# Performance work log

Hardware: AMD Instinct MI355X
Metric: run time of the kernel (lower is better)

## Reference

```python
import jax, jax.numpy as jnp
import numpy as np

D = 768           # input_dim == slot_dim
H, DH = 8, 64     # encoder attention heads / head dim (x-transformers defaults)
INNER = 4 * D     # ff_mult=4 GLU inner dim
EPS = 1e-8
N_ITERS = 3
SCALE = D ** -0.5


def _ln(x, g, b):
    m = jnp.mean(x, axis=-1, keepdims=True)
    v = jnp.var(x, axis=-1, keepdims=True)
    return (x - m) / jnp.sqrt(v + 1e-5) * g + b


def setup_inputs() -> dict:
    key = jax.random.key(0)
    ks = jax.random.split(key, 16)
    w = lambda i, shape, s=0.02: jax.random.normal(ks[i], shape, jnp.float32) * s
    return dict(
        x=jax.random.normal(ks[0], (32, 1024, D), jnp.float32),
        noise=jax.random.normal(ks[1], (32, 16, D), jnp.float32),
        init_mu=jax.random.normal(ks[2], (D,), jnp.float32),
        init_log_sigma=w(3, (D,), 0.05),
        Wk=w(4, (D, D)), Wv=w(5, (D, D)), Wq=w(6, (D, D)),
        ni_g=jnp.ones(D), ni_b=jnp.zeros(D),       # norm_input
        ns_g=jnp.ones(D), ns_b=jnp.zeros(D),       # norm_slots
        nica_g=jnp.ones(D), nica_b=jnp.zeros(D),   # norm_ica
        ln1_g=jnp.ones(D), ln1_b=jnp.zeros(D),     # encoder attn pre-norm
        Wq_a=w(7, (D, H * DH)), Wk_a=w(8, (D, H * DH)),
        Wv_a=w(9, (D, H * DH)), Wo_a=w(10, (H * DH, D)),
        ln2_g=jnp.ones(D), ln2_b=jnp.zeros(D),     # encoder ff pre-norm
        W1=w(11, (D, 2 * INNER)), W2=w(12, (INNER, D)),
        lnf_g=jnp.ones(D), lnf_b=jnp.zeros(D),     # encoder final norm
    )


def _inv_cross_attn(q, k, v):
    # softmax over the SLOT axis (dim i), then renormalize over keys j
    dots = jnp.einsum('bid,bjd->bij', q, k) * SCALE
    attn = jax.nn.softmax(dots, axis=1) + EPS
    attn = attn / jnp.sum(attn, axis=-1, keepdims=True)
    updates = jnp.einsum('bjd,bij->bid', v, attn)
    return updates, attn


def _encoder(h, ln1_g, ln1_b, Wq_a, Wk_a, Wv_a, Wo_a, ln2_g, ln2_b, W1, W2, lnf_g, lnf_b):
    b, n, _ = h.shape
    a = _ln(h, ln1_g, ln1_b)
    q = (a @ Wq_a).reshape(b, n, H, DH)
    k = (a @ Wk_a).reshape(b, n, H, DH)
    v = (a @ Wv_a).reshape(b, n, H, DH)
    scores = jnp.einsum('bihd,bjhd->bhij', q, k) * (DH ** -0.5)
    p = jax.nn.softmax(scores, axis=-1)
    o = jnp.einsum('bhij,bjhd->bihd', p, v).reshape(b, n, H * DH)
    h = h + o @ Wo_a
    f = _ln(h, ln2_g, ln2_b)
    u, g = jnp.split(f @ W1, 2, axis=-1)
    h = h + (u * jax.nn.silu(g)) @ W2
    return _ln(h, lnf_g, lnf_b)


def reference(x, noise, init_mu, init_log_sigma, Wk, Wv, Wq,
              ni_g, ni_b, ns_g, ns_b, nica_g, nica_b,
              ln1_g, ln1_b, Wq_a, Wk_a, Wv_a, Wo_a,
              ln2_g, ln2_b, W1, W2, lnf_g, lnf_b):
    xn = _ln(x, ni_g, ni_b)
    k = xn @ Wk
    v = xn @ Wv
    slots = init_mu + jnp.exp(init_log_sigma) * noise  # [b, n_slots, d]

    def step(slots):
        q = _ln(slots, ns_g, ns_b) @ Wq
        updates, attn = _inv_cross_attn(q, k, v)
        slots = _ln(slots + updates, nica_g, nica_b)
        slots = _encoder(slots, ln1_g, ln1_b, Wq_a, Wk_a, Wv_a, Wo_a,
                         ln2_g, ln2_b, W1, W2, lnf_g, lnf_b)
        return slots, attn

    for _ in range(N_ITERS):
        slots, _ = step(slots)
    slots, attn = step(slots)
    attn_map = jnp.transpose(attn, (0, 2, 1))  # b n hw -> b hw n
    return slots, attn_map
```

## Files before the change

### kernel.cpp

```cpp
#include <hip/hip_runtime.h>
#include <hip/hip_bf16.h>
#include <stdint.h>

typedef _Float16 f16;
typedef __attribute__((ext_vector_type(8))) _Float16 f16x8;
typedef __attribute__((ext_vector_type(4))) _Float16 f16x4;
typedef __attribute__((ext_vector_type(4))) float f32x4;

#define GLOBAL_AS __attribute__((address_space(1)))
#define LDS_AS __attribute__((address_space(3)))

#define D_DIM 768
#define NTOK 1024
#define NSLOT 16
#define NB 32
#define NTOT (NB*NTOK)
#define HDIM 512
#define INNER 3072
#define SCALE_D 0.03608439182435161f
#define SCALE_H 0.125f

template<int OUT>
__global__ __launch_bounds__(256) void mgemm64_k(
    const f16* __restrict__ A, const f16* __restrict__ Bt,
    void* __restrict__ Cout, int M, int N, int K, int Kc)
{
  __shared__ __align__(16) f16 As[64*128];
  __shared__ __align__(16) f16 Bs[64*128];
  const int tid = threadIdx.x;
  const int lane = tid & 63;
  const int wave = tid >> 6;
  const int m0 = blockIdx.x*64, n0 = blockIdx.y*64;
  const int kbeg = blockIdx.z * Kc;
  const int wm = (wave>>1)*32, wn = (wave&1)*32;
  const int quad = lane>>4, l16 = lane&15;

  const int sr = tid>>2;
  const int sc = (tid&3)*8;
  const f16* gA = A  + (size_t)(m0+sr)*K + kbeg + sc;
  const f16* gB = Bt + (size_t)(n0+sr)*K + kbeg + sc;
  LDS_AS f16* lA = (LDS_AS f16*)&As[(size_t)tid*8];
  LDS_AS f16* lB = (LDS_AS f16*)&Bs[(size_t)tid*8];

  const f16* fA0 = &As[(wm + l16)*32 + quad*8];
  const f16* fB0 = &Bs[(wn + l16)*32 + quad*8];

  f32x4 acc[2][2] = {};

  for (int k0 = 0; k0 < Kc; k0 += 128){
    #pragma unroll
    for (int p=0;p<4;++p){
      __builtin_amdgcn_global_load_lds((const GLOBAL_AS void*)(gA + k0 + p*32),
                                       (LDS_AS void*)(lA + (size_t)p*2048), 16, 0, 0);
      __builtin_amdgcn_global_load_lds((const GLOBAL_AS void*)(gB + k0 + p*32),
                                       (LDS_AS void*)(lB + (size_t)p*2048), 16, 0, 0);
    }
    __syncthreads();
    #pragma unroll
    for (int p=0;p<4;++p){
      f16x8 a0 = *(const f16x8*)(fA0 + p*2048);
      f16x8 a1 = *(const f16x8*)(fA0 + p*2048 + 16*32);
      f16x8 b0 = *(const f16x8*)(fB0 + p*2048);
      f16x8 b1 = *(const f16x8*)(fB0 + p*2048 + 16*32);
      acc[0][0] = __builtin_amdgcn_mfma_f32_16x16x32_f16(a0,b0,acc[0][0],0,0,0);
      acc[0][1] = __builtin_amdgcn_mfma_f32_16x16x32_f16(a0,b1,acc[0][1],0,0,0);
      acc[1][0] = __builtin_amdgcn_mfma_f32_16x16x32_f16(a1,b0,acc[1][0],0,0,0);
      acc[1][1] = __builtin_amdgcn_mfma_f32_16x16x32_f16(a1,b1,acc[1][1],0,0,0);
    }
    __syncthreads();
  }
  #pragma unroll
  for (int mt=0;mt<2;++mt){
    #pragma unroll
    for (int nt=0;nt<2;++nt){
      int gm = m0 + wm + mt*16 + quad*4;
      int gn = n0 + wn + nt*16 + l16;
      #pragma unroll
      for (int r=0;r<4;++r){
        float c = acc[mt][nt][r];
        size_t idx = (size_t)(gm+r)*N + gn;
        if (OUT==0)      ((float*)Cout)[idx] = c;
        else if (OUT==1) ((f16*)Cout)[idx] = (f16)c;
        else             atomicAdd(&((float*)Cout)[idx], c);
      }
    }
  }
}

__global__ __launch_bounds__(256) void w1glu_k(
    const f16* __restrict__ A, const f16* __restrict__ W1T,
    f16* __restrict__ act, int M)
{
  __shared__ __align__(16) f16 As[64*128];
  __shared__ __align__(16) f16 Bu[64*128];
  __shared__ __align__(16) f16 Bg[64*128];
  const int K = 768;
  const int tid = threadIdx.x;
  const int lane = tid & 63;
  const int wave = tid >> 6;
  const int m0 = blockIdx.x*64, n0 = blockIdx.y*64;
  const int wm = (wave>>1)*32, wn = (wave&1)*32;
  const int quad = lane>>4, l16 = lane&15;

  const int sr = tid>>2;
  const int sc = (tid&3)*8;
  const f16* gA  = A   + (size_t)(m0+sr)*K + sc;
  const f16* gBu = W1T + (size_t)(n0+sr)*K + sc;
  const f16* gBg = W1T + (size_t)(3072+n0+sr)*K + sc;
  LDS_AS f16* lA  = (LDS_AS f16*)&As[(size_t)tid*8];
  LDS_AS f16* lBu = (LDS_AS f16*)&Bu[(size_t)tid*8];
  LDS_AS f16* lBg = (LDS_AS f16*)&Bg[(size_t)tid*8];

  const f16* fA0 = &As[(wm + l16)*32 + quad*8];
  const f16* fU0 = &Bu[(wn + l16)*32 + quad*8];
  const f16* fG0 = &Bg[(wn + l16)*32 + quad*8];

  f32x4 accU[2][2] = {};
  f32x4 accG[2][2] = {};

  for (int k0 = 0; k0 < K; k0 += 128){
    #pragma unroll
    for (int p=0;p<4;++p){
      __builtin_amdgcn_global_load_lds((const GLOBAL_AS void*)(gA  + k0 + p*32),
                                       (LDS_AS void*)(lA  + (size_t)p*2048), 16, 0, 0);
      __builtin_amdgcn_global_load_lds((const GLOBAL_AS void*)(gBu + k0 + p*32),
                                       (LDS_AS void*)(lBu + (size_t)p*2048), 16, 0, 0);
      __builtin_amdgcn_global_load_lds((const GLOBAL_AS void*)(gBg + k0 + p*32),
                                       (LDS_AS void*)(lBg + (size_t)p*2048), 16, 0, 0);
    }
    __syncthreads();
    #pragma unroll
    for (int p=0;p<4;++p){
      f16x8 a0 = *(const f16x8*)(fA0 + p*2048);
      f16x8 a1 = *(const f16x8*)(fA0 + p*2048 + 16*32);
      f16x8 u0 = *(const f16x8*)(fU0 + p*2048);
      f16x8 u1 = *(const f16x8*)(fU0 + p*2048 + 16*32);
      f16x8 g0 = *(const f16x8*)(fG0 + p*2048);
      f16x8 g1 = *(const f16x8*)(fG0 + p*2048 + 16*32);
      accU[0][0] = __builtin_amdgcn_mfma_f32_16x16x32_f16(a0,u0,accU[0][0],0,0,0);
      accU[0][1] = __builtin_amdgcn_mfma_f32_16x16x32_f16(a0,u1,accU[0][1],0,0,0);
      accU[1][0] = __builtin_amdgcn_mfma_f32_16x16x32_f16(a1,u0,accU[1][0],0,0,0);
      accU[1][1] = __builtin_amdgcn_mfma_f32_16x16x32_f16(a1,u1,accU[1][1],0,0,0);
      accG[0][0] = __builtin_amdgcn_mfma_f32_16x16x32_f16(a0,g0,accG[0][0],0,0,0);
      accG[0][1] = __builtin_amdgcn_mfma_f32_16x16x32_f16(a0,g1,accG[0][1],0,0,0);
      accG[1][0] = __builtin_amdgcn_mfma_f32_16x16x32_f16(a1,g0,accG[1][0],0,0,0);
      accG[1][1] = __builtin_amdgcn_mfma_f32_16x16x32_f16(a1,g1,accG[1][1],0,0,0);
    }
    __syncthreads();
  }
  #pragma unroll
  for (int mt=0;mt<2;++mt){
    #pragma unroll
    for (int nt=0;nt<2;++nt){
      int gm = m0 + wm + mt*16 + quad*4;
      int gn = n0 + wn + nt*16 + l16;
      #pragma unroll
      for (int r=0;r<4;++r){
        float u = accU[mt][nt][r];
        float g = accG[mt][nt][r];
        float sg = g / (1.0f + __expf(-g));
        act[(size_t)(gm+r)*INNER + gn] = (f16)(u*sg);
      }
    }
  }
}

__global__ __launch_bounds__(256) void dots_k(
    const f16* __restrict__ Q,
    const f16* __restrict__ Xn,
    f16* __restrict__ attn,
    float* __restrict__ rsPart)
{
  __shared__ __align__(16) f16 qf[16*768];
  __shared__ __align__(16) f16 ks[64*128];
  __shared__ float rpart[4][16];
  const int b = blockIdx.x, jt = blockIdx.y;
  const int tid = threadIdx.x;
  const int lane = tid & 63;
  const int w = tid >> 6;
  const int quad = lane>>4, l16 = lane&15;

  #pragma unroll
  for (int c=0;c<6;++c){
    int p = c*256 + tid;
    int ki = p >> 6, qd = (p >> 4) & 3, rw = p & 15;
    f16x8 v = *(const f16x8*)(Q + ((size_t)(b*NSLOT+rw))*D_DIM + ki*32 + qd*8);
    *(f16x8*)&qf[(size_t)p*8] = v;
  }

  const f16* gK = Xn + ((size_t)(b*NTOK + jt*64 + (tid>>2)))*D_DIM + (tid&3)*8;
  LDS_AS f16* lK = (LDS_AS f16*)&ks[(size_t)tid*8];

  f32x4 acc = {};
  for (int it=0; it<6; ++it){
    #pragma unroll
    for (int p=0;p<4;++p)
      __builtin_amdgcn_global_load_lds((const GLOBAL_AS void*)(gK + it*128 + p*32),
                                       (LDS_AS void*)(lK + (size_t)p*2048), 16, 0, 0);
    __syncthreads();
    #pragma unroll
    for (int p=0;p<4;++p){
      f16x8 a  = *(const f16x8*)&qf[(((size_t)(it*4+p)*4 + quad)*16 + l16)*8];
      f16x8 bf = *(const f16x8*)&ks[(size_t)p*2048 + (w*16+l16)*32 + quad*8];
      acc = __builtin_amdgcn_mfma_f32_16x16x32_f16(a, bf, acc, 0, 0, 0);
    }
    __syncthreads();
  }

  float v0 = acc[0]*SCALE_D, v1 = acc[1]*SCALE_D, v2 = acc[2]*SCALE_D, v3 = acc[3]*SCALE_D;
  float mx = fmaxf(fmaxf(v0,v1), fmaxf(v2,v3));
  mx = fmaxf(mx, __shfl_xor(mx, 16));
  mx = fmaxf(mx, __shfl_xor(mx, 32));
  float e0 = __expf(v0-mx), e1 = __expf(v1-mx), e2 = __expf(v2-mx), e3 = __expf(v3-mx);
  float s = e0+e1+e2+e3;
  s += __shfl_xor(s, 16);
  s += __shfl_xor(s, 32);
  float inv = 1.0f/s;
  float a0 = e0*inv + 1e-8f, a1 = e1*inv + 1e-8f, a2 = e2*inv + 1e-8f, a3 = e3*inv + 1e-8f;

  int jcol = jt*64 + w*16 + l16;
  int ibase = b*NSLOT + quad*4;
  attn[(size_t)(ibase+0)*NTOK + jcol] = (f16)a0;
  attn[(size_t)(ibase+1)*NTOK + jcol] = (f16)a1;
  attn[(size_t)(ibase+2)*NTOK + jcol] = (f16)a2;
  attn[(size_t)(ibase+3)*NTOK + jcol] = (f16)a3;

  float t0=a0, t1=a1, t2=a2, t3=a3;
  #pragma unroll
  for (int m=1;m<16;m<<=1){
    t0 += __shfl_xor(t0, m);
    t1 += __shfl_xor(t1, m);
    t2 += __shfl_xor(t2, m);
    t3 += __shfl_xor(t3, m);
  }
  if (l16 == 0){
    rpart[w][quad*4+0] = t0;
    rpart[w][quad*4+1] = t1;
    rpart[w][quad*4+2] = t2;
    rpart[w][quad*4+3] = t3;
  }
  __syncthreads();
  if (tid < 16){
    float ss = rpart[0][tid] + rpart[1][tid] + rpart[2][tid] + rpart[3][tid];
    rsPart[(size_t)((b*16 + jt)<<4) + tid] = ss;
  }
}

__global__ __launch_bounds__(256) void attnv_k(
    const f16* __restrict__ attn,
    const float* __restrict__ rsPart,
    const f16* __restrict__ XnT,
    f16* __restrict__ t_out)
{
  __shared__ __align__(16) f16 Asl[16*128];
  __shared__ __align__(16) f16 Bsl[64*128];
  __shared__ float rsum[16];
  const int b = blockIdx.x, d0 = blockIdx.y*64;
  const int tid = threadIdx.x;
  const int lane = tid & 63;
  const int w = tid >> 6;
  const int quad = lane>>4, l16 = lane&15;

  if (tid < 16){
    float s = 0.f;
    #pragma unroll
    for (int jt=0;jt<16;++jt) s += rsPart[(size_t)((b*16 + jt)<<4) + tid];
    rsum[tid] = s;
  }

  const int pa = tid>>6, ta = tid&63;
  const f16* gA = attn + ((size_t)(b*NSLOT + (ta>>2)))*NTOK + pa*32 + (ta&3)*8;
  LDS_AS f16* lA = (LDS_AS f16*)&Asl[(size_t)pa*512 + ta*8];
  const f16* gB = XnT + ((size_t)(d0 + (tid>>2)))*NTOT + b*NTOK + (tid&3)*8;
  LDS_AS f16* lB = (LDS_AS f16*)&Bsl[(size_t)tid*8];

  f32x4 acc = {};
  for (int it=0; it<8; ++it){
    __builtin_amdgcn_global_load_lds((const GLOBAL_AS void*)(gA + it*128),
                                     (LDS_AS void*)lA, 16, 0, 0);
    #pragma unroll
    for (int p=0;p<4;++p)
      __builtin_amdgcn_global_load_lds((const GLOBAL_AS void*)(gB + it*128 + p*32),
                                       (LDS_AS void*)(lB + (size_t)p*2048), 16, 0, 0);
    __syncthreads();
    #pragma unroll
    for (int p=0;p<4;++p){
      f16x8 a  = *(const f16x8*)&Asl[(size_t)p*512 + l16*32 + quad*8];
      f16x8 bf = *(const f16x8*)&Bsl[(size_t)p*2048 + (w*16+l16)*32 + quad*8];
      acc = __builtin_amdgcn_mfma_f32_16x16x32_f16(a, bf, acc, 0, 0, 0);
    }
    __syncthreads();
  }
  int dcol = d0 + w*16 + l16;
  #pragma unroll
  for (int r=0;r<4;++r){
    int i = quad*4 + r;
    t_out[(size_t)(b*NSLOT + i)*D_DIM + dcol] = (f16)(acc[r] / rsum[i]);
  }
}

__global__ __launch_bounds__(256) void lnw_k(
    const float* __restrict__ X,
    const float* __restrict__ g, const float* __restrict__ bb,
    f16* __restrict__ out)
{
  const int lane = threadIdx.x & 63;
  const size_t row = (size_t)blockIdx.x*4 + (threadIdx.x>>6);
  const float* x = X + row*D_DIM;
  float4 v[3]; float s=0.f, ss=0.f;
  #pragma unroll
  for (int t=0;t<3;++t){
    v[t] = *(const float4*)(x + lane*4 + t*256);
    s  += v[t].x+v[t].y+v[t].z+v[t].w;
    ss += v[t].x*v[t].x+v[t].y*v[t].y+v[t].z*v[t].z+v[t].w*v[t].w;
  }
  #pragma unroll
  for (int m=1;m<64;m<<=1){ s += __shfl_xor(s,m); ss += __shfl_xor(ss,m); }
  float mean = s*(1.0f/768.0f);
  float inv  = rsqrtf(ss*(1.0f/768.0f) - mean*mean + 1e-5f);
  #pragma unroll
  for (int t=0;t<3;++t){
    int c0 = lane*4 + t*256;
    float4 gg = *(const float4*)(g + c0);
    float4 bv = *(const float4*)(bb + c0);
    f16x4 h4;
    h4.x = (f16)((v[t].x-mean)*inv*gg.x + bv.x);
    h4.y = (f16)((v[t].y-mean)*inv*gg.y + bv.y);
    h4.z = (f16)((v[t].z-mean)*inv*gg.z + bv.z);
    h4.w = (f16)((v[t].w-mean)*inv*gg.w + bv.w);
    *(f16x4*)(out + row*D_DIM + c0) = h4;
  }
}

template<bool ADD>
__global__ __launch_bounds__(256) void lnlnw_k(
    const float* __restrict__ X, const float* __restrict__ X2,
    const float* __restrict__ g1, const float* __restrict__ b1,
    const float* __restrict__ g2, const float* __restrict__ b2,
    float* __restrict__ out1, f16* __restrict__ out2)
{
  const int lane = threadIdx.x & 63;
  const size_t row = (size_t)blockIdx.x*4 + (threadIdx.x>>6);
  const float* x = X + row*D_DIM;
  const float* x2 = X2 + row*D_DIM;
  float4 v[3]; float s=0.f, ss=0.f;
  #pragma unroll
  for (int t=0;t<3;++t){
    int c0 = lane*4 + t*256;
    float4 a = *(const float4*)(x + c0);
    if (ADD){
      float4 b = *(const float4*)(x2 + c0);
      a.x+=b.x; a.y+=b.y; a.z+=b.z; a.w+=b.w;
    }
    v[t]=a;
    s  += v[t].x+v[t].y+v[t].z+v[t].w;
    ss += v[t].x*v[t].x+v[t].y*v[t].y+v[t].z*v[t].z+v[t].w*v[t].w;
  }
  #pragma unroll
  for (int m=1;m<64;m<<=1){ s += __shfl_xor(s,m); ss += __shfl_xor(ss,m); }
  float mean = s*(1.0f/768.0f);
  float inv  = rsqrtf(ss*(1.0f/768.0f) - mean*mean + 1e-5f);
  float y[3][4]; float s2=0.f, ss2=0.f;
  #pragma unroll
  for (int t=0;t<3;++t){
    int c0 = lane*4 + t*256;
    float4 gg = *(const float4*)(g1 + c0);
    float4 bv = *(const float4*)(b1 + c0);
    y[t][0] = (v[t].x-mean)*inv*gg.x + bv.x;
    y[t][1] = (v[t].y-mean)*inv*gg.y + bv.y;
    y[t][2] = (v[t].z-mean)*inv*gg.z + bv.z;
    y[t][3] = (v[t].w-mean)*inv*gg.w + bv.w;
    float4 o = { y[t][0], y[t][1], y[t][2], y[t][3] };
    *(float4*)(out1 + row*D_DIM + c0) = o;
    s2  += y[t][0]+y[t][1]+y[t][2]+y[t][3];
    ss2 += y[t][0]*y[t][0]+y[t][1]*y[t][1]+y[t][2]*y[t][2]+y[t][3]*y[t][3];
  }
  #pragma unroll
  for (int m=1;m<64;m<<=1){ s2 += __shfl_xor(s2,m); ss2 += __shfl_xor(ss2,m); }
  float mean2 = s2*(1.0f/768.0f);
  float inv2  = rsqrtf(ss2*(1.0f/768.0f) - mean2*mean2 + 1e-5f);
  #pragma unroll
  for (int t=0;t<3;++t){
    int c0 = lane*4 + t*256;
    float4 gg = *(const float4*)(g2 + c0);
    float4 bv = *(const float4*)(b2 + c0);
    f16x4 h4;
    h4.x = (f16)((y[t][0]-mean2)*inv2*gg.x + bv.x);
    h4.y = (f16)((y[t][1]-mean2)*inv2*gg.y + bv.y);
    h4.z = (f16)((y[t][2]-mean2)*inv2*gg.z + bv.z);
    h4.w = (f16)((y[t][3]-mean2)*inv2*gg.w + bv.w);
    *(f16x4*)(out2 + row*D_DIM + c0) = h4;
  }
}

__global__ __launch_bounds__(256) void slotsinit_k(
    const float* __restrict__ noise, const float* __restrict__ mu,
    const float* __restrict__ ls,
    const float* __restrict__ nsg, const float* __restrict__ nsb,
    float* __restrict__ slots, f16* __restrict__ tmp2)
{
  const int lane = threadIdx.x & 63;
  const size_t row = (size_t)blockIdx.x*4 + (threadIdx.x>>6);
  float4 v[3]; float s=0.f, ss=0.f;
  #pragma unroll
  for (int t=0;t<3;++t){
    int c0 = lane*4 + t*256;
    float4 nz = *(const float4*)(noise + row*D_DIM + c0);
    float4 m4 = *(const float4*)(mu + c0);
    float4 l4 = *(const float4*)(ls + c0);
    v[t].x = m4.x + __expf(l4.x)*nz.x;
    v[t].y = m4.y + __expf(l4.y)*nz.y;
    v[t].z = m4.z + __expf(l4.z)*nz.z;
    v[t].w = m4.w + __expf(l4.w)*nz.w;
    *(float4*)(slots + row*D_DIM + c0) = v[t];
    s  += v[t].x+v[t].y+v[t].z+v[t].w;
    ss += v[t].x*v[t].x+v[t].y*v[t].y+v[t].z*v[t].z+v[t].w*v[t].w;
  }
  #pragma unroll
  for (int m=1;m<64;m<<=1){ s += __shfl_xor(s,m); ss += __shfl_xor(ss,m); }
  float mean = s*(1.0f/768.0f);
  float inv  = rsqrtf(ss*(1.0f/768.0f) - mean*mean + 1e-5f);
  #pragma unroll
  for (int t=0;t<3;++t){
    int c0 = lane*4 + t*256;
    float4 gg = *(const float4*)(nsg + c0);
    float4 bv = *(const float4*)(nsb + c0);
    f16x4 h4;
    h4.x = (f16)((v[t].x-mean)*inv*gg.x + bv.x);
    h4.y = (f16)((v[t].y-mean)*inv*gg.y + bv.y);
    h4.z = (f16)((v[t].z-mean)*inv*gg.z + bv.z);
    h4.w = (f16)((v[t].w-mean)*inv*gg.w + bv.w);
    *(f16x4*)(tmp2 + row*D_DIM + c0) = h4;
  }
}

__global__ __launch_bounds__(256) void encattn_k(
    const f16* __restrict__ QA, const f16* __restrict__ KA,
    const f16* __restrict__ VA, int QSTR,
    f16* __restrict__ O)
{
  __shared__ float qs[16][68], ks[16][68], vs[16][68], ps[16][20];
  const int b = blockIdx.x, h = blockIdx.y;
  const int tid = threadIdx.x;
  {
    int i = tid>>4, dd=(tid&15)*4;
    size_t base = ((size_t)(b*NSLOT+i))*QSTR + h*64 + dd;
    f16x4 uq = *(const f16x4*)(QA + base);
    f16x4 uk = *(const f16x4*)(KA + base);
    f16x4 uv = *(const f16x4*)(VA + base);
    float4 fq = { (float)uq.x, (float)uq.y, (float)uq.z, (float)uq.w };
    float4 fk = { (float)uk.x, (float)uk.y, (float)uk.z, (float)uk.w };
    float4 fv = { (float)uv.x, (float)uv.y, (float)uv.z, (float)uv.w };
    *(float4*)&qs[i][dd]=fq; *(float4*)&ks[i][dd]=fk; *(float4*)&vs[i][dd]=fv;
  }
  __syncthreads();
  {
    int i = tid>>4, j = tid&15;
    float s=0.f;
    #pragma unroll 8
    for (int d=0; d<64; ++d) s += qs[i][d]*ks[j][d];
    ps[i][j] = s*SCALE_H;
  }
  __syncthreads();
  if (tid < 16){
    int i = tid;
    float mx=-1e30f;
    #pragma unroll
    for (int j=0;j<16;++j) mx = fmaxf(mx, ps[i][j]);
    float sm=0.f;
    #pragma unroll
    for (int j=0;j<16;++j){ float e=__expf(ps[i][j]-mx); ps[i][j]=e; sm+=e; }
    float inv=1.0f/sm;
    #pragma unroll
    for (int j=0;j<16;++j) ps[i][j]*=inv;
  }
  __syncthreads();
  {
    int i = tid>>4, dq=(tid&15)*4;
    float a0=0,a1=0,a2=0,a3=0;
    #pragma unroll
    for (int j=0;j<16;++j){
      float p = ps[i][j];
      a0+=p*vs[j][dq+0]; a1+=p*vs[j][dq+1]; a2+=p*vs[j][dq+2]; a3+=p*vs[j][dq+3];
    }
    size_t base = ((size_t)(b*NSLOT+i))*HDIM + h*64 + dq;
    O[base+0]=(f16)a0; O[base+1]=(f16)a1; O[base+2]=(f16)a2; O[base+3]=(f16)a3;
  }
}

__global__ __launch_bounds__(256) void transp_k(
    const f16* __restrict__ in, f16* __restrict__ out, int R, int C)
{
  __shared__ f16 T[64][72];
  const int m0 = blockIdx.x*64, d0 = blockIdx.y*64;
  const int tid = threadIdx.x;
  {
    int r = tid>>2, c = (tid&3)*16;
    const f16* p = in + (size_t)(m0+r)*C + d0 + c;
    *(f16x8*)&T[r][c]   = *(const f16x8*)p;
    *(f16x8*)&T[r][c+8] = *(const f16x8*)(p+8);
  }
  __syncthreads();
  {
    int dd = tid>>2, mq = (tid&3)*16;
    f16 v[16];
    #pragma unroll
    for (int e=0;e<16;++e) v[e] = T[mq+e][dd];
    f16* p = out + (size_t)(d0+dd)*R + m0 + mq;
    *(f16x8*)p     = *(f16x8*)&v[0];
    *(f16x8*)(p+8) = *(f16x8*)&v[8];
  }
}

__global__ __launch_bounds__(256) void prep_k(
    const float* __restrict__ Wv,   const float* __restrict__ Wq_a,
    const float* __restrict__ Wk_a, const float* __restrict__ Wv_a,
    const float* __restrict__ Wo_a, const float* __restrict__ W1,
    const float* __restrict__ W2,   const float* __restrict__ Wk,
    const float* __restrict__ Wq,
    f16* __restrict__ WvT, f16* __restrict__ WqkvT, f16* __restrict__ WoaT,
    f16* __restrict__ W1T, f16* __restrict__ W2T,
    f16* __restrict__ Wkf, f16* __restrict__ Wqf)
{
  __shared__ float t[32][33];
  int bid = blockIdx.x;
  const float* src; f16* dst; int R, C; bool tr = true;
  if      (bid < 576)  {              src=Wv;   dst=WvT;             R=768;  C=768; }
  else if (bid < 960)  { bid-=576;    src=Wq_a; dst=WqkvT;           R=768;  C=512; }
  else if (bid < 1344) { bid-=960;    src=Wk_a; dst=WqkvT+512*768;   R=768;  C=512; }
  else if (bid < 1728) { bid-=1344;   src=Wv_a; dst=WqkvT+1024*768;  R=768;  C=512; }
  else if (bid < 2112) { bid-=1728;   src=Wo_a; dst=WoaT;            R=512;  C=768; }
  else if (bid < 6720) { bid-=2112;   src=W1;   dst=W1T;             R=768;  C=6144; }
  else if (bid < 9024) { bid-=6720;   src=W2;   dst=W2T;             R=3072; C=768; }
  else if (bid < 9600) { bid-=9024;   src=Wk;   dst=Wkf;             R=768;  C=768; tr=false; }
  else                 { bid-=9600;   src=Wq;   dst=Wqf;             R=768;  C=768; tr=false; }
  const int tpr = C/32;
  const int r0 = (bid / tpr)*32, c0 = (bid % tpr)*32;
  const int lc = threadIdx.x & 31, g8 = threadIdx.x >> 5;
  if (tr){
    #pragma unroll
    for (int s=0;s<4;++s){
      int r = g8*4 + s;
      t[r][lc] = src[(size_t)(r0+r)*C + c0+lc];
    }
    __syncthreads();
    #pragma unroll
    for (int s=0;s<4;++s){
      int c = g8*4 + s;
      dst[(size_t)(c0+c)*R + r0+lc] = (f16)t[lc][c];
    }
  } else {
    #pragma unroll
    for (int s=0;s<4;++s){
      int r = g8*4 + s;
      dst[(size_t)(r0+r)*C + c0+lc] = (f16)src[(size_t)(r0+r)*C + c0+lc];
    }
  }
}

__global__ __launch_bounds__(256) void attnout_k(
    const f16* __restrict__ attn, const float* __restrict__ rsPart,
    float* __restrict__ out)
{
  __shared__ float rsum[16];
  const int bid = blockIdx.x, tid = threadIdx.x;
  const int b = bid >> 6;
  if (tid < 16){
    float s = 0.f;
    #pragma unroll
    for (int jt=0;jt<16;++jt) s += rsPart[(size_t)((b*16+jt)<<4) + tid];
    rsum[tid] = s;
  }
  __syncthreads();
  int idx = bid*256 + tid;
  int i = idx & 15;
  int j = (idx >> 4) & 1023;
  out[idx] = (float)attn[((size_t)(b*NSLOT)+i)*NTOK + j] / rsum[i];
}

extern "C" void kernel_launch(void* const* d_in, const int* in_sizes, int n_in,
                              void* d_out, int out_size, void* d_ws, size_t ws_size,
                              hipStream_t stream) {
  const float* x        = (const float*)d_in[0];
  const float* noise    = (const float*)d_in[1];
  const float* init_mu  = (const float*)d_in[2];
  const float* init_ls  = (const float*)d_in[3];
  const float* Wk       = (const float*)d_in[4];
  const float* Wv       = (const float*)d_in[5];
  const float* Wq       = (const float*)d_in[6];
  const float* ni_g     = (const float*)d_in[7];
  const float* ni_b     = (const float*)d_in[8];
  const float* ns_g     = (const float*)d_in[9];
  const float* ns_b     = (const float*)d_in[10];
  const float* nica_g   = (const float*)d_in[11];
  const float* nica_b   = (const float*)d_in[12];
  const float* ln1_g    = (const float*)d_in[13];
  const float* ln1_b    = (const float*)d_in[14];
  const float* Wq_a     = (const float*)d_in[15];
  const float* Wk_a     = (const float*)d_in[16];
  const float* Wv_a     = (const float*)d_in[17];
  const float* Wo_a     = (const float*)d_in[18];
  const float* ln2_g    = (const float*)d_in[19];
  const float* ln2_b    = (const float*)d_in[20];
  const float* W1       = (const float*)d_in[21];
  const float* W2       = (const float*)d_in[22];
  const float* lnf_g    = (const float*)d_in[23];
  const float* lnf_b    = (const float*)d_in[24];

  char* w = (char*)d_ws;
  size_t off = 0;
  auto alloc = [&](size_t bytes)->char*{
    char* p = w + off; off += (bytes + 255) & ~(size_t)255; return p;
  };
  f16* xn_h  = (f16*)alloc((size_t)NTOT*D_DIM*2);
  f16* xnT_h = (f16*)alloc((size_t)D_DIM*NTOT*2);
  f16* Wkf   = (f16*)alloc((size_t)768*768*2);
  f16* Wqf   = (f16*)alloc((size_t)768*768*2);
  f16* BtQK  = (f16*)alloc((size_t)768*768*2);
  f16* WvT   = (f16*)alloc((size_t)768*768*2);
  f16* WqkvT = (f16*)alloc((size_t)1536*768*2);
  f16* WoaT  = (f16*)alloc((size_t)768*512*2);
  f16* W1T   = (f16*)alloc((size_t)6144*768*2);
  f16* W2T   = (f16*)alloc((size_t)768*3072*2);
  float* slots = (float*)alloc(512*768*4);
  float* hbuf  = (float*)alloc(512*768*4);
  float* upd   = (float*)alloc(512*768*4);
  f16* tmp_h  = (f16*)alloc(512*768*2);
  f16* tmp2_h = (f16*)alloc(512*768*2);
  f16* q_h    = (f16*)alloc(512*768*2);
  f16* t_h    = (f16*)alloc(512*768*2);
  f16* qkv_h  = (f16*)alloc((size_t)512*1536*2);
  f16* o_h    = (f16*)alloc(512*512*2);
  f16* act_h  = (f16*)alloc((size_t)512*3072*2);
  f16* attn_h = (f16*)alloc((size_t)NB*NSLOT*NTOK*2);
  float* rsPart = (float*)alloc((size_t)32*16*16*4);

  prep_k<<<10176, 256, 0, stream>>>(Wv, Wq_a, Wk_a, Wv_a, Wo_a, W1, W2, Wk, Wq,
                                    WvT, WqkvT, WoaT, W1T, W2T, Wkf, Wqf);

  mgemm64_k<1><<<dim3(12, 12, 1), 256, 0, stream>>>(Wkf, Wqf, BtQK, 768, 768, 768, 768);

  lnw_k<<<NTOT/4, 256, 0, stream>>>(x, ni_g, ni_b, xn_h);
  transp_k<<<dim3(NTOT/64, D_DIM/64), 256, 0, stream>>>(xn_h, xnT_h, NTOT, D_DIM);

  slotsinit_k<<<128, 256, 0, stream>>>(noise, init_mu, init_ls, ns_g, ns_b,
                                       slots, tmp2_h);

  for (int it=0; it<4; ++it){
    mgemm64_k<1><<<dim3(8, 12, 1), 256, 0, stream>>>(tmp2_h, BtQK, q_h, 512, 768, 768, 768);
    dots_k<<<dim3(NB, 16), 256, 0, stream>>>(q_h, xn_h, attn_h, rsPart);
    attnv_k<<<dim3(NB, 12), 256, 0, stream>>>(attn_h, rsPart, xnT_h, t_h);
    mgemm64_k<0><<<dim3(8, 12, 1), 256, 0, stream>>>(t_h, WvT, upd, 512, 768, 768, 768);
    lnlnw_k<true><<<128, 256, 0, stream>>>(slots, upd, nica_g, nica_b, ln1_g, ln1_b,
                                           hbuf, tmp_h);
    mgemm64_k<1><<<dim3(8, 24, 1), 256, 0, stream>>>(tmp_h, WqkvT, qkv_h, 512, 1536, 768, 768);
    encattn_k<<<dim3(NB, 8), 256, 0, stream>>>(qkv_h, qkv_h + 512, qkv_h + 1024, 1536, o_h);
    mgemm64_k<2><<<dim3(8, 12, 2), 256, 0, stream>>>(o_h, WoaT, hbuf, 512, 768, 512, 256);
    lnw_k<<<128, 256, 0, stream>>>(hbuf, ln2_g, ln2_b, tmp_h);
    w1glu_k<<<dim3(8, 48), 256, 0, stream>>>(tmp_h, W1T, act_h, 512);
    mgemm64_k<2><<<dim3(8, 12, 4), 256, 0, stream>>>(act_h, W2T, hbuf, 512, 768, 3072, 768);
    float* out1 = (it==3) ? (float*)d_out : slots;
    lnlnw_k<false><<<128, 256, 0, stream>>>(hbuf, nullptr, lnf_g, lnf_b, ns_g, ns_b,
                                            out1, tmp2_h);
  }

  attnout_k<<<NB*NTOK*NSLOT/256, 256, 0, stream>>>(attn_h, rsPart, (float*)d_out + 512*768);
}
```

Baseline: 627.9 us.

## Replace atomic split-K with partial buffers reduced in consumer kernels

All the small slot-side GEMMs now run split-K. Each K-slice writes its fp32 partial to its own buffer instead of using atomicAdd. The partials are summed inside the kernels that consume them (dots, layernorm, encoder attention), which spreads 512-row GEMMs over more blocks and drops the atomics. The cost is extra fp32 partial traffic, more workspace, and changed rounding because the q/qkv intermediates are now fp32 sums rather than fp16.

After: 634.8 us. Within noise of the previous version (+1.1%).

```diff
diff --git a/kernel.cpp b/kernel.cpp
--- a/kernel.cpp
+++ b/kernel.cpp
@@ -17,6 +17,7 @@
 #define NTOT (NB*NTOK)
 #define HDIM 512
 #define INNER 3072
+#define SLOTSZ (512*768)
 #define SCALE_D 0.03608439182435161f
 #define SCALE_H 0.125f
 
@@ -69,6 +70,7 @@
     }
     __syncthreads();
   }
+  const size_t zoff = (size_t)blockIdx.z * M * N;
   #pragma unroll
   for (int mt=0;mt<2;++mt){
     #pragma unroll
@@ -79,9 +81,8 @@
       for (int r=0;r<4;++r){
         float c = acc[mt][nt][r];
         size_t idx = (size_t)(gm+r)*N + gn;
-        if (OUT==0)      ((float*)Cout)[idx] = c;
-        else if (OUT==1) ((f16*)Cout)[idx] = (f16)c;
-        else             atomicAdd(&((float*)Cout)[idx], c);
+        if (OUT==1) ((f16*)Cout)[idx] = (f16)c;
+        else        ((float*)Cout)[zoff + idx] = c;
       }
     }
   }
@@ -166,7 +167,8 @@
 }
 
 __global__ __launch_bounds__(256) void dots_k(
-    const f16* __restrict__ Q,
+    const float* __restrict__ Q0, const float* __restrict__ Q1,
+    const float* __restrict__ Q2,
     const f16* __restrict__ Xn,
     f16* __restrict__ attn,
     float* __restrict__ rsPart)
@@ -184,7 +186,15 @@
   for (int c=0;c<6;++c){
     int p = c*256 + tid;
     int ki = p >> 6, qd = (p >> 4) & 3, rw = p & 15;
-    f16x8 v = *(const f16x8*)(Q + ((size_t)(b*NSLOT+rw))*D_DIM + ki*32 + qd*8);
+    size_t qo = ((size_t)(b*NSLOT+rw))*D_DIM + ki*32 + qd*8;
+    float4 a0 = *(const float4*)(Q0+qo), a1 = *(const float4*)(Q0+qo+4);
+    float4 b0 = *(const float4*)(Q1+qo), b1 = *(const float4*)(Q1+qo+4);
+    float4 c0 = *(const float4*)(Q2+qo), c1 = *(const float4*)(Q2+qo+4);
+    f16x8 v;
+    v[0]=(f16)(a0.x+b0.x+c0.x); v[1]=(f16)(a0.y+b0.y+c0.y);
+    v[2]=(f16)(a0.z+b0.z+c0.z); v[3]=(f16)(a0.w+b0.w+c0.w);
+    v[4]=(f16)(a1.x+b1.x+c1.x); v[5]=(f16)(a1.y+b1.y+c1.y);
+    v[6]=(f16)(a1.z+b1.z+c1.z); v[7]=(f16)(a1.w+b1.w+c1.w);
     *(f16x8*)&qf[(size_t)p*8] = v;
   }
 
@@ -332,27 +342,26 @@
   }
 }
 
-template<bool ADD>
-__global__ __launch_bounds__(256) void lnlnw_k(
-    const float* __restrict__ X, const float* __restrict__ X2,
+__global__ __launch_bounds__(256) void lnln_res_k(
+    const float* __restrict__ S,  const float* __restrict__ U0,
+    const float* __restrict__ U1, const float* __restrict__ U2,
     const float* __restrict__ g1, const float* __restrict__ b1,
     const float* __restrict__ g2, const float* __restrict__ b2,
     float* __restrict__ out1, f16* __restrict__ out2)
 {
   const int lane = threadIdx.x & 63;
   const size_t row = (size_t)blockIdx.x*4 + (threadIdx.x>>6);
-  const float* x = X + row*D_DIM;
-  const float* x2 = X2 + row*D_DIM;
+  const size_t ro = row*D_DIM;
   float4 v[3]; float s=0.f, ss=0.f;
   #pragma unroll
   for (int t=0;t<3;++t){
     int c0 = lane*4 + t*256;
-    float4 a = *(const float4*)(x + c0);
-    if (ADD){
-      float4 b = *(const float4*)(x2 + c0);
-      a.x+=b.x; a.y+=b.y; a.z+=b.z; a.w+=b.w;
-    }
-    v[t]=a;
+    float4 a = *(const float4*)(S + ro + c0);
+    float4 b = *(const float4*)(U0 + ro + c0);
+    float4 c = *(const float4*)(U1 + ro + c0);
+    float4 d = *(const float4*)(U2 + ro + c0);
+    v[t].x = a.x+b.x+c.x+d.x; v[t].y = a.y+b.y+c.y+d.y;
+    v[t].z = a.z+b.z+c.z+d.z; v[t].w = a.w+b.w+c.w+d.w;
     s  += v[t].x+v[t].y+v[t].z+v[t].w;
     ss += v[t].x*v[t].x+v[t].y*v[t].y+v[t].z*v[t].z+v[t].w*v[t].w;
   }
@@ -371,7 +380,7 @@
     y[t][2] = (v[t].z-mean)*inv*gg.z + bv.z;
     y[t][3] = (v[t].w-mean)*inv*gg.w + bv.w;
     float4 o = { y[t][0], y[t][1], y[t][2], y[t][3] };
-    *(float4*)(out1 + row*D_DIM + c0) = o;
+    *(float4*)(out1 + ro + c0) = o;
     s2  += y[t][0]+y[t][1]+y[t][2]+y[t][3];
     ss2 += y[t][0]*y[t][0]+y[t][1]*y[t][1]+y[t][2]*y[t][2]+y[t][3]*y[t][3];
   }
@@ -389,7 +398,107 @@
     h4.y = (f16)((y[t][1]-mean2)*inv2*gg.y + bv.y);
     h4.z = (f16)((y[t][2]-mean2)*inv2*gg.z + bv.z);
     h4.w = (f16)((y[t][3]-mean2)*inv2*gg.w + bv.w);
-    *(f16x4*)(out2 + row*D_DIM + c0) = h4;
+    *(f16x4*)(out2 + ro + c0) = h4;
+  }
+}
+
+__global__ __launch_bounds__(256) void lnadd3_k(
+    const float* __restrict__ H1, const float* __restrict__ O0,
+    const float* __restrict__ O1,
+    const float* __restrict__ g, const float* __restrict__ bb,
+    float* __restrict__ h2, f16* __restrict__ out)
+{
+  const int lane = threadIdx.x & 63;
+  const size_t row = (size_t)blockIdx.x*4 + (threadIdx.x>>6);
+  const size_t ro = row*D_DIM;
+  float4 v[3]; float s=0.f, ss=0.f;
+  #pragma unroll
+  for (int t=0;t<3;++t){
+    int c0 = lane*4 + t*256;
+    float4 a = *(const float4*)(H1 + ro + c0);
+    float4 b = *(const float4*)(O0 + ro + c0);
+    float4 c = *(const float4*)(O1 + ro + c0);
+    v[t].x = a.x+b.x+c.x; v[t].y = a.y+b.y+c.y;
+    v[t].z = a.z+b.z+c.z; v[t].w = a.w+b.w+c.w;
+    *(float4*)(h2 + ro + c0) = v[t];
+    s  += v[t].x+v[t].y+v[t].z+v[t].w;
+    ss += v[t].x*v[t].x+v[t].y*v[t].y+v[t].z*v[t].z+v[t].w*v[t].w;
+  }
+  #pragma unroll
+  for (int m=1;m<64;m<<=1){ s += __shfl_xor(s,m); ss += __shfl_xor(ss,m); }
+  float mean = s*(1.0f/768.0f);
+  float inv  = rsqrtf(ss*(1.0f/768.0f) - mean*mean + 1e-5f);
+  #pragma unroll
+  for (int t=0;t<3;++t){
+    int c0 = lane*4 + t*256;
+    float4 gg = *(const float4*)(g + c0);
+    float4 bv = *(const float4*)(bb + c0);
+    f16x4 h4;
+    h4.x = (f16)((v[t].x-mean)*inv*gg.x + bv.x);
+    h4.y = (f16)((v[t].y-mean)*inv*gg.y + bv.y);
+    h4.z = (f16)((v[t].z-mean)*inv*gg.z + bv.z);
+    h4.w = (f16)((v[t].w-mean)*inv*gg.w + bv.w);
+    *(f16x4*)(out + ro + c0) = h4;
+  }
+}
+
+__global__ __launch_bounds__(256) void lnfin_k(
+    const float* __restrict__ H2, const float* __restrict__ Wb,
+    const float* __restrict__ g1, const float* __restrict__ b1,
+    const float* __restrict__ g2, const float* __restrict__ b2,
+    float* __restrict__ out1, f16* __restrict__ out2)
+{
+  const int lane = threadIdx.x & 63;
+  const size_t row = (size_t)blockIdx.x*4 + (threadIdx.x>>6);
+  const size_t ro = row*D_DIM;
+  float4 v[3]; float s=0.f, ss=0.f;
+  #pragma unroll
+  for (int t=0;t<3;++t){
+    int c0 = lane*4 + t*256;
+    float4 a = *(const float4*)(H2 + ro + c0);
+    #pragma unroll
+    for (int z=0;z<8;++z){
+      float4 b = *(const float4*)(Wb + (size_t)z*SLOTSZ + ro + c0);
+      a.x+=b.x; a.y+=b.y; a.z+=b.z; a.w+=b.w;
+    }
+    v[t]=a;
+    s  += v[t].x+v[t].y+v[t].z+v[t].w;
+    ss += v[t].x*v[t].x+v[t].y*v[t].y+v[t].z*v[t].z+v[t].w*v[t].w;
+  }
+  #pragma unroll
+  for (int m=1;m<64;m<<=1){ s += __shfl_xor(s,m); ss += __shfl_xor(ss,m); }
+  float mean = s*(1.0f/768.0f);
+  float inv  = rsqrtf(ss*(1.0f/768.0f) - mean*mean + 1e-5f);
+  float y[3][4]; float s2=0.f, ss2=0.f;
+  #pragma unroll
+  for (int t=0;t<3;++t){
+    int c0 = lane*4 + t*256;
+    float4 gg = *(const float4*)(g1 + c0);
+    float4 bv = *(const float4*)(b1 + c0);
+    y[t][0] = (v[t].x-mean)*inv*gg.x + bv.x;
+    y[t][1] = (v[t].y-mean)*inv*gg.y + bv.y;
+    y[t][2] = (v[t].z-mean)*inv*gg.z + bv.z;
+    y[t][3] = (v[t].w-mean)*inv*gg.w + bv.w;
+    float4 o = { y[t][0], y[t][1], y[t][2], y[t][3] };
+    *(float4*)(out1 + ro + c0) = o;
+    s2  += y[t][0]+y[t][1]+y[t][2]+y[t][3];
+    ss2 += y[t][0]*y[t][0]+y[t][1]*y[t][1]+y[t][2]*y[t][2]+y[t][3]*y[t][3];
+  }
+  #pragma unroll
+  for (int m=1;m<64;m<<=1){ s2 += __shfl_xor(s2,m); ss2 += __shfl_xor(ss2,m); }
+  float mean2 = s2*(1.0f/768.0f);
+  float inv2  = rsqrtf(ss2*(1.0f/768.0f) - mean2*mean2 + 1e-5f);
+  #pragma unroll
+  for (int t=0;t<3;++t){
+    int c0 = lane*4 + t*256;
+    float4 gg = *(const float4*)(g2 + c0);
+    float4 bv = *(const float4*)(b2 + c0);
+    f16x4 h4;
+    h4.x = (f16)((y[t][0]-mean2)*inv2*gg.x + bv.x);
+    h4.y = (f16)((y[t][1]-mean2)*inv2*gg.y + bv.y);
+    h4.z = (f16)((y[t][2]-mean2)*inv2*gg.z + bv.z);
+    h4.w = (f16)((y[t][3]-mean2)*inv2*gg.w + bv.w);
+    *(f16x4*)(out2 + ro + c0) = h4;
   }
 }
 
@@ -435,8 +544,8 @@
 }
 
 __global__ __launch_bounds__(256) void encattn_k(
-    const f16* __restrict__ QA, const f16* __restrict__ KA,
-    const f16* __restrict__ VA, int QSTR,
+    const float* __restrict__ A0, const float* __restrict__ A1,
+    const float* __restrict__ A2,
     f16* __restrict__ O)
 {
   __shared__ float qs[16][68], ks[16][68], vs[16][68], ps[16][20];
@@ -444,13 +553,19 @@
   const int tid = threadIdx.x;
   {
     int i = tid>>4, dd=(tid&15)*4;
-    size_t base = ((size_t)(b*NSLOT+i))*QSTR + h*64 + dd;
-    f16x4 uq = *(const f16x4*)(QA + base);
-    f16x4 uk = *(const f16x4*)(KA + base);
-    f16x4 uv = *(const f16x4*)(VA + base);
-    float4 fq = { (float)uq.x, (float)uq.y, (float)uq.z, (float)uq.w };
-    float4 fk = { (float)uk.x, (float)uk.y, (float)uk.z, (float)uk.w };
-    float4 fv = { (float)uv.x, (float)uv.y, (float)uv.z, (float)uv.w };
+    size_t base = ((size_t)(b*NSLOT+i))*1536 + h*64 + dd;
+    float4 q0 = *(const float4*)(A0+base);
+    float4 q1 = *(const float4*)(A1+base);
+    float4 q2 = *(const float4*)(A2+base);
+    float4 k0 = *(const float4*)(A0+base+512);
+    float4 k1 = *(const float4*)(A1+base+512);
+    float4 k2 = *(const float4*)(A2+base+512);
+    float4 u0 = *(const float4*)(A0+base+1024);
+    float4 u1 = *(const float4*)(A1+base+1024);
+    float4 u2 = *(const float4*)(A2+base+1024);
+    float4 fq = { q0.x+q1.x+q2.x, q0.y+q1.y+q2.y, q0.z+q1.z+q2.z, q0.w+q1.w+q2.w };
+    float4 fk = { k0.x+k1.x+k2.x, k0.y+k1.y+k2.y, k0.z+k1.z+k2.z, k0.w+k1.w+k2.w };
+    float4 fv = { u0.x+u1.x+u2.x, u0.y+u1.y+u2.y, u0.z+u1.z+u2.z, u0.w+u1.w+u2.w };
     *(float4*)&qs[i][dd]=fq; *(float4*)&ks[i][dd]=fk; *(float4*)&vs[i][dd]=fv;
   }
   __syncthreads();
@@ -622,14 +737,17 @@
   f16* WoaT  = (f16*)alloc((size_t)768*512*2);
   f16* W1T   = (f16*)alloc((size_t)6144*768*2);
   f16* W2T   = (f16*)alloc((size_t)768*3072*2);
-  float* slots = (float*)alloc(512*768*4);
-  float* hbuf  = (float*)alloc(512*768*4);
-  float* upd   = (float*)alloc(512*768*4);
-  f16* tmp_h  = (f16*)alloc(512*768*2);
-  f16* tmp2_h = (f16*)alloc(512*768*2);
-  f16* q_h    = (f16*)alloc(512*768*2);
-  f16* t_h    = (f16*)alloc(512*768*2);
-  f16* qkv_h  = (f16*)alloc((size_t)512*1536*2);
+  float* slots = (float*)alloc(SLOTSZ*4);
+  float* hbuf  = (float*)alloc(SLOTSZ*4);
+  float* h2buf = (float*)alloc(SLOTSZ*4);
+  float* q32   = (float*)alloc((size_t)3*SLOTSZ*4);
+  float* upd3  = (float*)alloc((size_t)3*SLOTSZ*4);
+  float* qkv32 = (float*)alloc((size_t)3*512*1536*4);
+  float* oo    = (float*)alloc((size_t)2*SLOTSZ*4);
+  float* ww    = (float*)alloc((size_t)8*SLOTSZ*4);
+  f16* tmp_h  = (f16*)alloc(SLOTSZ*2);
+  f16* tmp2_h = (f16*)alloc(SLOTSZ*2);
+  f16* t_h    = (f16*)alloc(SLOTSZ*2);
   f16* o_h    = (f16*)alloc(512*512*2);
   f16* act_h  = (f16*)alloc((size_t)512*3072*2);
   f16* attn_h = (f16*)alloc((size_t)NB*NSLOT*NTOK*2);
@@ -647,21 +765,22 @@
                                        slots, tmp2_h);
 
   for (int it=0; it<4; ++it){
-    mgemm64_k<1><<<dim3(8, 12, 1), 256, 0, stream>>>(tmp2_h, BtQK, q_h, 512, 768, 768, 768);
-    dots_k<<<dim3(NB, 16), 256, 0, stream>>>(q_h, xn_h, attn_h, rsPart);
+    mgemm64_k<3><<<dim3(8, 12, 3), 256, 0, stream>>>(tmp2_h, BtQK, q32, 512, 768, 768, 256);
+    dots_k<<<dim3(NB, 16), 256, 0, stream>>>(q32, q32+SLOTSZ, q32+2*SLOTSZ,
+                                             xn_h, attn_h, rsPart);
     attnv_k<<<dim3(NB, 12), 256, 0, stream>>>(attn_h, rsPart, xnT_h, t_h);
-    mgemm64_k<0><<<dim3(8, 12, 1), 256, 0, stream>>>(t_h, WvT, upd, 512, 768, 768, 768);
-    lnlnw_k<true><<<128, 256, 0, stream>>>(slots, upd, nica_g, nica_b, ln1_g, ln1_b,
-                                           hbuf, tmp_h);
-    mgemm64_k<1><<<dim3(8, 24, 1), 256, 0, stream>>>(tmp_h, WqkvT, qkv_h, 512, 1536, 768, 768);
-    encattn_k<<<dim3(NB, 8), 256, 0, stream>>>(qkv_h, qkv_h + 512, qkv_h + 1024, 1536, o_h);
-    mgemm64_k<2><<<dim3(8, 12, 2), 256, 0, stream>>>(o_h, WoaT, hbuf, 512, 768, 512, 256);
-    lnw_k<<<128, 256, 0, stream>>>(hbuf, ln2_g, ln2_b, tmp_h);
+    mgemm64_k<3><<<dim3(8, 12, 3), 256, 0, stream>>>(t_h, WvT, upd3, 512, 768, 768, 256);
+    lnln_res_k<<<128, 256, 0, stream>>>(slots, upd3, upd3+SLOTSZ, upd3+2*SLOTSZ,
+                                        nica_g, nica_b, ln1_g, ln1_b, hbuf, tmp_h);
+    mgemm64_k<3><<<dim3(8, 24, 3), 256, 0, stream>>>(tmp_h, WqkvT, qkv32, 512, 1536, 768, 256);
+    encattn_k<<<dim3(NB, 8), 256, 0, stream>>>(qkv32, qkv32+512*1536, qkv32+2*512*1536, o_h);
+    mgemm64_k<3><<<dim3(8, 12, 2), 256, 0, stream>>>(o_h, WoaT, oo, 512, 768, 512, 256);
+    lnadd3_k<<<128, 256, 0, stream>>>(hbuf, oo, oo+SLOTSZ, ln2_g, ln2_b, h2buf, tmp_h);
     w1glu_k<<<dim3(8, 48), 256, 0, stream>>>(tmp_h, W1T, act_h, 512);
-    mgemm64_k<2><<<dim3(8, 12, 4), 256, 0, stream>>>(act_h, W2T, hbuf, 512, 768, 3072, 768);
+    mgemm64_k<3><<<dim3(8, 12, 8), 256, 0, stream>>>(act_h, W2T, ww, 512, 768, 3072, 384);
     float* out1 = (it==3) ? (float*)d_out : slots;
-    lnlnw_k<false><<<128, 256, 0, stream>>>(hbuf, nullptr, lnf_g, lnf_b, ns_g, ns_b,
-                                            out1, tmp2_h);
+    lnfin_k<<<128, 256, 0, stream>>>(h2buf, ww, lnf_g, lnf_b, ns_g, ns_b,
+                                     out1, tmp2_h);
   }
 
   attnout_k<<<NB*NTOK*NSLOT/256, 256, 0, stream>>>(attn_h, rsPart, (float*)d_out + 512*768);
```
